# Optimization experiments

Measured on AMD Instinct MI355X. Metric: run time of the kernel, lower is better.

Reference implementation:

```python
import jax, jax.numpy as jnp
import numpy as np

N_NODES = 100000
N_EDGES = 1600000
IN_DIM = 256
OUT_DIM = 128


def setup_inputs() -> dict:
    key = jax.random.key(0)
    k1, k2, k3, k4, k5 = jax.random.split(key, 5)
    h = jax.random.normal(k1, (N_NODES, IN_DIM), dtype=jnp.float32)
    # xavier_normal-ish scales for the two weight matrices
    W = jax.random.normal(k2, (IN_DIM, OUT_DIM), dtype=jnp.float32) * (2.0 / np.sqrt(IN_DIM + OUT_DIM))
    a = jax.random.normal(k3, (2 * OUT_DIM,), dtype=jnp.float32) * (2.0 / np.sqrt(2 * OUT_DIM + 1))
    src = jax.random.randint(k4, (N_EDGES,), 0, N_NODES, dtype=jnp.int32)
    dst = jax.random.randint(k5, (N_EDGES,), 0, N_NODES, dtype=jnp.int32)
    return {"h": h, "W": W, "a": a, "src": src, "dst": dst}


def reference(h, W, a, src, dst):
    n = h.shape[0]
    d = W.shape[1]
    z = h @ W  # [N, out_dim]
    # attn_fc([z_src || z_dst]) == z_src @ a[:d] + z_dst @ a[d:]
    el = z @ a[:d]  # [N]
    er = z @ a[d:]  # [N]
    e = jax.nn.leaky_relu(el[src] + er[dst])  # [E], torch default slope 0.01
    # per-destination (segment) softmax, numerically stable
    seg_max = jax.ops.segment_max(e, dst, num_segments=n)
    e_exp = jnp.exp(e - seg_max[dst])
    denom = jax.ops.segment_sum(e_exp, dst, num_segments=n)
    alpha = e_exp / denom[dst]  # [E]
    # weighted scatter-sum of source z into destinations
    h_out = jax.ops.segment_sum(alpha[:, None] * z[src], dst, num_segments=n)
    return h_out
```

## Files before the change

kernel.cpp:

```cpp
#include <hip/hip_runtime.h>
#include <cstdint>
#include <cstddef>

#define N_NODES 100000
#define N_EDGES 1600000
#define IN_DIM  256
#define OUT_DIM 128

#define BSHIFT 6
#define BNODES 64
#define NBUCK  1563
#define BCAP   1600
#define CNTMAX 1408
#define EPB    2048
#define PGB    2346

typedef __attribute__((ext_vector_type(8))) short bf16x8;
typedef __attribute__((ext_vector_type(4))) float f32x4;

__device__ __forceinline__ unsigned bf16rn(float f) {
    unsigned u = __float_as_uint(f);
    return (u + 0x7FFFu + ((u >> 16) & 1u)) >> 16;
}

__global__ __launch_bounds__(256) void setup_k(
    const float* __restrict__ W, unsigned short* __restrict__ w16s,
    int* __restrict__ bucket_cursor)
{
    int t = blockIdx.x * blockDim.x + threadIdx.x;
    if (t < NBUCK) bucket_cursor[t] = 0;
    if (t >= IN_DIM * OUT_DIM) return;
    int j  = t & 7;
    int n  = (t >> 3) & 15;
    int q  = (t >> 7) & 3;
    int c  = (t >> 9) & 7;
    int kc = t >> 12;
    int k   = kc * 32 + q * 8 + j;
    int dim = (c >> 1) * 32 + n * 2 + (c & 1);
    w16s[t] = (unsigned short)bf16rn(W[k * OUT_DIM + dim]);
}

__global__ __launch_bounds__(256, 3) void pg_k(
    const int* __restrict__ src, const int* __restrict__ dst,
    int* __restrict__ bucket_cursor, unsigned* __restrict__ ebuf,
    const float* __restrict__ h, const unsigned short* __restrict__ w16s,
    const float* __restrict__ a,
    unsigned short* __restrict__ z16, float* __restrict__ el, float* __restrict__ er)
{
    __shared__ int hist[NBUCK];
    __shared__ int gbaseL[NBUCK];
    const int t   = threadIdx.x;
    const int bid = blockIdx.x;

    if ((bid % 3) == 2) {
        const int pid = bid / 3;
        for (int i = t; i < NBUCK; i += 256) hist[i] = 0;
        __syncthreads();

        const int e0 = pid * EPB;
        int bucks[8], ranks[8];
        unsigned pk[8];
        #pragma unroll
        for (int k = 0; k < 8; ++k) {
            int e = e0 + k * 256 + t;
            bucks[k] = -1;
            if (e < N_EDGES) {
                int s = src[e], d = dst[e];
                int b = d >> BSHIFT;
                bucks[k] = b;
                ranks[k] = atomicAdd(&hist[b], 1);
                pk[k] = ((unsigned)s << BSHIFT) | (unsigned)(d & (BNODES - 1));
            }
        }
        __syncthreads();
        for (int i = t; i < NBUCK; i += 256) {
            int hc = hist[i];
            gbaseL[i] = hc ? atomicAdd(&bucket_cursor[i], hc) : 0;
        }
        __syncthreads();
        #pragma unroll
        for (int k = 0; k < 8; ++k)
            if (bucks[k] >= 0) {
                int p = gbaseL[bucks[k]] + ranks[k];
                if (p < BCAP)
                    ebuf[(size_t)bucks[k] * BCAP + p] = pk[k];
            }
        return;
    }

    const int gid  = (bid / 3) * 2 + (bid % 3);
    const int n0   = gid * 64;
    if (n0 >= N_NODES) return;
    const int w    = t >> 6;
    const int lane = t & 63;
    const int q    = lane >> 4;
    const int col  = lane & 15;

    int row  = n0 + w * 16 + col;
    int lrow = (row < N_NODES) ? row : (N_NODES - 1);
    const float* hp = h + (size_t)lrow * IN_DIM + q * 8;

    f32x4 acc[8];
    #pragma unroll
    for (int c = 0; c < 8; ++c) acc[c] = (f32x4){0.f, 0.f, 0.f, 0.f};

    #pragma unroll
    for (int kc = 0; kc < 8; ++kc) {
        float4 v0 = *(const float4*)(hp + kc * 32);
        float4 v1 = *(const float4*)(hp + kc * 32 + 4);
        bf16x8 af;
        af[0] = (short)bf16rn(v0.x); af[1] = (short)bf16rn(v0.y);
        af[2] = (short)bf16rn(v0.z); af[3] = (short)bf16rn(v0.w);
        af[4] = (short)bf16rn(v1.x); af[5] = (short)bf16rn(v1.y);
        af[6] = (short)bf16rn(v1.z); af[7] = (short)bf16rn(v1.w);
        #pragma unroll
        for (int c = 0; c < 8; ++c) {
            bf16x8 bfr = *(const bf16x8*)&w16s[((((kc * 8 + c) * 4 + q) * 16) + col) * 8];
            acc[c] = __builtin_amdgcn_mfma_f32_16x16x32_bf16(af, bfr, acc[c], 0, 0, 0);
        }
    }

    float aL[8], aR[8];
    #pragma unroll
    for (int c = 0; c < 8; ++c) {
        int dim = (c >> 1) * 32 + col * 2 + (c & 1);
        aL[c] = a[dim];
        aR[c] = a[128 + dim];
    }
    #pragma unroll
    for (int r = 0; r < 4; ++r) {
        int node = n0 + w * 16 + q * 4 + r;
        float sl = 0.f, sr = 0.f;
        #pragma unroll
        for (int c = 0; c < 8; ++c) {
            sl += acc[c][r] * aL[c];
            sr += acc[c][r] * aR[c];
        }
        #pragma unroll
        for (int o = 1; o < 16; o <<= 1) {
            sl += __shfl_xor(sl, o, 64);
            sr += __shfl_xor(sr, o, 64);
        }
        if (node < N_NODES) {
            #pragma unroll
            for (int g = 0; g < 4; ++g) {
                unsigned u = bf16rn(acc[2 * g][r]) | (bf16rn(acc[2 * g + 1][r]) << 16);
                ((unsigned*)z16)[(size_t)node * 64 + g * 16 + col] = u;
            }
            if (col == 0) { el[node] = sl; er[node] = sr; }
        }
    }
}

__global__ __launch_bounds__(512, 8) void bn_k(
    const int* __restrict__ bucket_cursor, const unsigned* __restrict__ ebuf,
    const float* __restrict__ el, const float* __restrict__ er,
    const unsigned* __restrict__ z16, float* __restrict__ out)
{
    __shared__ float erL[2 * BNODES];
    __shared__ int   degA[BNODES], offA[BNODES];
    __shared__ int   degB[BNODES], offB[BNODES];
    __shared__ unsigned long long wsA[BCAP], wsB[BCAP];

    const int blk = blockIdx.x;
    const int t   = threadIdx.x;
    const int bA  = blk * 2;
    const int bB  = blk * 2 + 1;
    const bool hasB = (bB < NBUCK);

    int cA = bucket_cursor[bA]; if (cA > CNTMAX) cA = CNTMAX;
    int cB = 0;
    if (hasB) { cB = bucket_cursor[bB]; if (cB > CNTMAX) cB = CNTMAX; }

    if (t < BNODES) { degA[t] = 0; degB[t] = 0; }
    if (t < 2 * BNODES) {
        int bucket = (t < BNODES) ? bA : bB;
        int n = bucket * BNODES + (t & (BNODES - 1));
        erL[t] = (bucket < NBUCK && n < N_NODES) ? er[n] : 0.f;
    }
    __syncthreads();

    const int iA = 4 * t;
    unsigned evsA[4] = {0u, 0u, 0u, 0u};
    float wA[4]; int rkA[4];
    if (iA < cA) {
        uint4 v = *(const uint4*)&ebuf[(size_t)bA * BCAP + iA];
        evsA[0] = v.x; evsA[1] = v.y; evsA[2] = v.z; evsA[3] = v.w;
    }
    {
        float eg[4];
        #pragma unroll
        for (int j = 0; j < 4; ++j)
            eg[j] = (iA + j < cA) ? el[evsA[j] >> BSHIFT] : 0.f;
        #pragma unroll
        for (int j = 0; j < 4; ++j) {
            if (iA + j < cA) {
                int ld = evsA[j] & (BNODES - 1);
                float e = eg[j] + erL[ld];
                e = (e > 0.f) ? e : 0.01f * e;
                wA[j]  = __expf(e);
                rkA[j] = atomicAdd(&degA[ld], 1);
            }
        }
    }
    __syncthreads();

    if (t < BNODES) {
        int d = degA[t], pd = (d + 3) & ~3, incl = pd;
        #pragma unroll
        for (int o = 1; o < 64; o <<= 1) {
            int x = __shfl_up(incl, o, 64);
            if (t >= o) incl += x;
        }
        offA[t] = incl - pd;
    }
    __syncthreads();

    #pragma unroll
    for (int j = 0; j < 4; ++j)
        if (iA + j < cA) {
            int ld = evsA[j] & (BNODES - 1);
            wsA[offA[ld] + rkA[j]] =
                ((unsigned long long)__float_as_uint(wA[j]) << 32) | (evsA[j] >> BSHIFT);
        }
    if (t < BNODES) {
        int d = degA[t], pd = (d + 3) & ~3, o = offA[t];
        for (int j = o + d; j < o + pd; ++j) wsA[j] = 0ull;
    }
    __syncthreads();

    unsigned evsB[4] = {0u, 0u, 0u, 0u};
    float wB[4]; int rkB[4];
    if (iA < cB) {
        uint4 v = *(const uint4*)&ebuf[(size_t)bB * BCAP + iA];
        evsB[0] = v.x; evsB[1] = v.y; evsB[2] = v.z; evsB[3] = v.w;
    }
    {
        float eg[4];
        #pragma unroll
        for (int j = 0; j < 4; ++j)
            eg[j] = (iA + j < cB) ? el[evsB[j] >> BSHIFT] : 0.f;
        #pragma unroll
        for (int j = 0; j < 4; ++j) {
            if (iA + j < cB) {
                int ld = evsB[j] & (BNODES - 1);
                float e = eg[j] + erL[BNODES + ld];
                e = (e > 0.f) ? e : 0.01f * e;
                wB[j]  = __expf(e);
                rkB[j] = atomicAdd(&degB[ld], 1);
            }
        }
    }

    const int wv   = t >> 6;
    const int lane = t & 63;
    #pragma unroll 1
    for (int k = 0; k < BNODES / 8; ++k) {
        int ln = wv * (BNODES / 8) + k;
        int n  = bA * BNODES + ln;
        if (n >= N_NODES) continue;
        int o   = offA[ln];
        int dl  = degA[ln];
        int pdl = (dl + 3) & ~3;
        float acc0 = 0.f, acc1 = 0.f, dsum = 0.f;
        #pragma unroll 2
        for (int i = o; i < o + pdl; i += 4) {
            unsigned long long e0 = wsA[i],     e1 = wsA[i + 1];
            unsigned long long e2 = wsA[i + 2], e3 = wsA[i + 3];
            float w0 = __uint_as_float((unsigned)(e0 >> 32));
            float w1 = __uint_as_float((unsigned)(e1 >> 32));
            float w2 = __uint_as_float((unsigned)(e2 >> 32));
            float w3 = __uint_as_float((unsigned)(e3 >> 32));
            unsigned q0 = z16[(size_t)(unsigned)e0 * 64 + lane];
            unsigned q1 = z16[(size_t)(unsigned)e1 * 64 + lane];
            unsigned q2 = z16[(size_t)(unsigned)e2 * 64 + lane];
            unsigned q3 = z16[(size_t)(unsigned)e3 * 64 + lane];
            acc0 += w0 * __uint_as_float(q0 << 16)
                  + w1 * __uint_as_float(q1 << 16)
                  + w2 * __uint_as_float(q2 << 16)
                  + w3 * __uint_as_float(q3 << 16);
            acc1 += w0 * __uint_as_float(q0 & 0xFFFF0000u)
                  + w1 * __uint_as_float(q1 & 0xFFFF0000u)
                  + w2 * __uint_as_float(q2 & 0xFFFF0000u)
                  + w3 * __uint_as_float(q3 & 0xFFFF0000u);
            dsum += w0 + w1 + w2 + w3;
        }
        if (pdl > 0) {
            float inv = 1.0f / dsum;
            acc0 *= inv; acc1 *= inv;
        }
        *(float2*)&out[(size_t)n * OUT_DIM + lane * 2] = make_float2(acc0, acc1);
    }
    __syncthreads();

    if (t < BNODES) {
        int d = degB[t], pd = (d + 3) & ~3, incl = pd;
        #pragma unroll
        for (int o = 1; o < 64; o <<= 1) {
            int x = __shfl_up(incl, o, 64);
            if (t >= o) incl += x;
        }
        offB[t] = incl - pd;
    }
    __syncthreads();

    #pragma unroll
    for (int j = 0; j < 4; ++j)
        if (iA + j < cB) {
            int ld = evsB[j] & (BNODES - 1);
            wsB[offB[ld] + rkB[j]] =
                ((unsigned long long)__float_as_uint(wB[j]) << 32) | (evsB[j] >> BSHIFT);
        }
    if (t < BNODES) {
        int d = degB[t], pd = (d + 3) & ~3, o = offB[t];
        for (int j = o + d; j < o + pd; ++j) wsB[j] = 0ull;
    }
    __syncthreads();

    if (hasB) {
        #pragma unroll 1
        for (int k = 0; k < BNODES / 8; ++k) {
            int ln = wv * (BNODES / 8) + k;
            int n  = bB * BNODES + ln;
            if (n >= N_NODES) continue;
            int o   = offB[ln];
            int dl  = degB[ln];
            int pdl = (dl + 3) & ~3;
            float acc0 = 0.f, acc1 = 0.f, dsum = 0.f;
            #pragma unroll 2
            for (int i = o; i < o + pdl; i += 4) {
                unsigned long long e0 = wsB[i],     e1 = wsB[i + 1];
                unsigned long long e2 = wsB[i + 2], e3 = wsB[i + 3];
                float w0 = __uint_as_float((unsigned)(e0 >> 32));
                float w1 = __uint_as_float((unsigned)(e1 >> 32));
                float w2 = __uint_as_float((unsigned)(e2 >> 32));
                float w3 = __uint_as_float((unsigned)(e3 >> 32));
                unsigned q0 = z16[(size_t)(unsigned)e0 * 64 + lane];
                unsigned q1 = z16[(size_t)(unsigned)e1 * 64 + lane];
                unsigned q2 = z16[(size_t)(unsigned)e2 * 64 + lane];
                unsigned q3 = z16[(size_t)(unsigned)e3 * 64 + lane];
                acc0 += w0 * __uint_as_float(q0 << 16)
                      + w1 * __uint_as_float(q1 << 16)
                      + w2 * __uint_as_float(q2 << 16)
                      + w3 * __uint_as_float(q3 << 16);
                acc1 += w0 * __uint_as_float(q0 & 0xFFFF0000u)
                      + w1 * __uint_as_float(q1 & 0xFFFF0000u)
                      + w2 * __uint_as_float(q2 & 0xFFFF0000u)
                      + w3 * __uint_as_float(q3 & 0xFFFF0000u);
                dsum += w0 + w1 + w2 + w3;
            }
            if (pdl > 0) {
                float inv = 1.0f / dsum;
                acc0 *= inv; acc1 *= inv;
            }
            *(float2*)&out[(size_t)n * OUT_DIM + lane * 2] = make_float2(acc0, acc1);
        }
    }
}

extern "C" void kernel_launch(void* const* d_in, const int* in_sizes, int n_in,
                              void* d_out, int out_size, void* d_ws, size_t ws_size,
                              hipStream_t stream)
{
    (void)in_sizes; (void)n_in; (void)out_size; (void)ws_size;
    const float* h = (const float*)d_in[0];
    const float* W = (const float*)d_in[1];
    const float* a = (const float*)d_in[2];
    const int* src = (const int*)d_in[3];
    const int* dst = (const int*)d_in[4];
    float* out = (float*)d_out;

    char* ws = (char*)d_ws;
    size_t off = 0;
    auto alloc = [&](size_t bytes) -> char* {
        char* p = ws + off;
        off += (bytes + 255) & ~(size_t)255;
        return p;
    };
    unsigned short* z16  = (unsigned short*)alloc((size_t)N_NODES * OUT_DIM * 2);
    unsigned short* w16s = (unsigned short*)alloc((size_t)IN_DIM * OUT_DIM * 2);
    float*    el        = (float*)   alloc((size_t)N_NODES * 4);
    float*    er        = (float*)   alloc((size_t)N_NODES * 4);
    int*      bucket_cursor = (int*) alloc((size_t)NBUCK * 4);
    unsigned* ebuf      = (unsigned*)alloc((size_t)NBUCK * BCAP * 4);

    setup_k<<<(IN_DIM * OUT_DIM + 255) / 256, 256, 0, stream>>>(W, w16s, bucket_cursor);
    pg_k<<<PGB, 256, 0, stream>>>(src, dst, bucket_cursor, ebuf,
                                  h, w16s, a, z16, el, er);
    bn_k<<<(NBUCK + 1) / 2, 512, 0, stream>>>(bucket_cursor, ebuf, el, er,
                                              (const unsigned*)z16, out);
}
```

Baseline: 287.6 us.

## Split fp32-to-bf16 h conversion from GEMM into separate pass before partitioning

The fused projection+partition kernel is replaced by a kernel that converts h to a bf16 copy, builds the edge buckets and converts W, followed by a separate GEMM kernel that reads the bf16 h and preloads all A fragments. The bucket cursor reset moves to a memset. The intent is to overlap the bandwidth-bound h conversion with edge partitioning and to let the GEMM load half the bytes with loads issued ahead of the MFMA chain. In exchange it adds an extra 51 MB write and read of h16, plus one more kernel launch.

```diff
diff --git a/kernel.cpp b/kernel.cpp
--- a/kernel.cpp
+++ b/kernel.cpp
@@ -13,7 +13,10 @@
 #define BCAP   1600
 #define CNTMAX 1408
 #define EPB    2048
-#define PGB    2346
+#define NH16   1564
+#define NPART  782
+#define NW16   128
+#define PHPB   (NH16 + NPART + NW16)
 
 typedef __attribute__((ext_vector_type(8))) short bf16x8;
 typedef __attribute__((ext_vector_type(4))) float f32x4;
@@ -23,34 +26,29 @@
     return (u + 0x7FFFu + ((u >> 16) & 1u)) >> 16;
 }
 
-__global__ __launch_bounds__(256) void setup_k(
-    const float* __restrict__ W, unsigned short* __restrict__ w16s,
-    int* __restrict__ bucket_cursor)
-{
-    int t = blockIdx.x * blockDim.x + threadIdx.x;
-    if (t < NBUCK) bucket_cursor[t] = 0;
-    if (t >= IN_DIM * OUT_DIM) return;
-    int j  = t & 7;
-    int n  = (t >> 3) & 15;
-    int q  = (t >> 7) & 3;
-    int c  = (t >> 9) & 7;
-    int kc = t >> 12;
-    int k   = kc * 32 + q * 8 + j;
-    int dim = (c >> 1) * 32 + n * 2 + (c & 1);
-    w16s[t] = (unsigned short)bf16rn(W[k * OUT_DIM + dim]);
-}
-
-__global__ __launch_bounds__(256, 3) void pg_k(
+__global__ __launch_bounds__(256) void php_k(
+    const float* __restrict__ h, unsigned short* __restrict__ h16,
     const int* __restrict__ src, const int* __restrict__ dst,
     int* __restrict__ bucket_cursor, unsigned* __restrict__ ebuf,
-    const float* __restrict__ h, const unsigned short* __restrict__ w16s,
-    const float* __restrict__ a,
-    unsigned short* __restrict__ z16, float* __restrict__ el, float* __restrict__ er)
+    const float* __restrict__ W, unsigned short* __restrict__ w16s)
 {
     __shared__ int hist[NBUCK];
     __shared__ int gbaseL[NBUCK];
     const int t   = threadIdx.x;
     const int bid = blockIdx.x;
+
+    if (bid >= NH16 + NPART) {
+        int tt = (bid - (NH16 + NPART)) * 256 + t;
+        int j  = tt & 7;
+        int n  = (tt >> 3) & 15;
+        int q  = (tt >> 7) & 3;
+        int c  = (tt >> 9) & 7;
+        int kc = tt >> 12;
+        int k   = kc * 32 + q * 8 + j;
+        int dim = (c >> 1) * 32 + n * 2 + (c & 1);
+        w16s[tt] = (unsigned short)bf16rn(W[k * OUT_DIM + dim]);
+        return;
+    }
 
     if ((bid % 3) == 2) {
         const int pid = bid / 3;
@@ -88,8 +86,31 @@
         return;
     }
 
-    const int gid  = (bid / 3) * 2 + (bid % 3);
-    const int n0   = gid * 64;
+    const int gid = (bid / 3) * 2 + (bid % 3);
+    #pragma unroll
+    for (int jj = 0; jj < 8; ++jj) {
+        size_t base = (size_t)gid * 16384 + jj * 2048 + t * 8;
+        if (base < (size_t)N_NODES * IN_DIM) {
+            float4 v0 = *(const float4*)&h[base];
+            float4 v1 = *(const float4*)&h[base + 4];
+            uint2 lo, hi;
+            lo.x = bf16rn(v0.x) | (bf16rn(v0.y) << 16);
+            lo.y = bf16rn(v0.z) | (bf16rn(v0.w) << 16);
+            hi.x = bf16rn(v1.x) | (bf16rn(v1.y) << 16);
+            hi.y = bf16rn(v1.z) | (bf16rn(v1.w) << 16);
+            *(uint2*)&h16[base]     = lo;
+            *(uint2*)&h16[base + 4] = hi;
+        }
+    }
+}
+
+__global__ __launch_bounds__(256, 3) void gemm_k(
+    const unsigned short* __restrict__ h16, const unsigned short* __restrict__ w16s,
+    const float* __restrict__ a,
+    unsigned short* __restrict__ z16, float* __restrict__ el, float* __restrict__ er)
+{
+    const int t    = threadIdx.x;
+    const int n0   = blockIdx.x * 64;
     if (n0 >= N_NODES) return;
     const int w    = t >> 6;
     const int lane = t & 63;
@@ -98,7 +119,12 @@
 
     int row  = n0 + w * 16 + col;
     int lrow = (row < N_NODES) ? row : (N_NODES - 1);
-    const float* hp = h + (size_t)lrow * IN_DIM + q * 8;
+    const unsigned short* hp = h16 + (size_t)lrow * IN_DIM + q * 8;
+
+    bf16x8 vh[8];
+    #pragma unroll
+    for (int kc = 0; kc < 8; ++kc)
+        vh[kc] = *(const bf16x8*)&hp[kc * 32];
 
     f32x4 acc[8];
     #pragma unroll
@@ -106,17 +132,10 @@
 
     #pragma unroll
     for (int kc = 0; kc < 8; ++kc) {
-        float4 v0 = *(const float4*)(hp + kc * 32);
-        float4 v1 = *(const float4*)(hp + kc * 32 + 4);
-        bf16x8 af;
-        af[0] = (short)bf16rn(v0.x); af[1] = (short)bf16rn(v0.y);
-        af[2] = (short)bf16rn(v0.z); af[3] = (short)bf16rn(v0.w);
-        af[4] = (short)bf16rn(v1.x); af[5] = (short)bf16rn(v1.y);
-        af[6] = (short)bf16rn(v1.z); af[7] = (short)bf16rn(v1.w);
         #pragma unroll
         for (int c = 0; c < 8; ++c) {
             bf16x8 bfr = *(const bf16x8*)&w16s[((((kc * 8 + c) * 4 + q) * 16) + col) * 8];
-            acc[c] = __builtin_amdgcn_mfma_f32_16x16x32_bf16(af, bfr, acc[c], 0, 0, 0);
+            acc[c] = __builtin_amdgcn_mfma_f32_16x16x32_bf16(vh[kc], bfr, acc[c], 0, 0, 0);
         }
     }
 
@@ -378,15 +397,16 @@
         return p;
     };
     unsigned short* z16  = (unsigned short*)alloc((size_t)N_NODES * OUT_DIM * 2);
+    unsigned short* h16  = (unsigned short*)alloc((size_t)N_NODES * IN_DIM * 2);
     unsigned short* w16s = (unsigned short*)alloc((size_t)IN_DIM * OUT_DIM * 2);
     float*    el        = (float*)   alloc((size_t)N_NODES * 4);
     float*    er        = (float*)   alloc((size_t)N_NODES * 4);
     int*      bucket_cursor = (int*) alloc((size_t)NBUCK * 4);
     unsigned* ebuf      = (unsigned*)alloc((size_t)NBUCK * BCAP * 4);
 
-    setup_k<<<(IN_DIM * OUT_DIM + 255) / 256, 256, 0, stream>>>(W, w16s, bucket_cursor);
-    pg_k<<<PGB, 256, 0, stream>>>(src, dst, bucket_cursor, ebuf,
-                                  h, w16s, a, z16, el, er);
+    hipMemsetAsync(bucket_cursor, 0, (size_t)NBUCK * 4, stream);
+    php_k<<<PHPB, 256, 0, stream>>>(h, h16, src, dst, bucket_cursor, ebuf, W, w16s);
+    gemm_k<<<1564, 256, 0, stream>>>(h16, w16s, a, z16, el, er);
     bn_k<<<(NBUCK + 1) / 2, 512, 0, stream>>>(bucket_cursor, ebuf, el, er,
                                               (const unsigned*)z16, out);
 }
```

Result: slower. 307.4 us (+6.9%).

## Split fused partition/GEMM kernel and stage bf16 weights in LDS

Applied to the files above, without the earlier changes.

Separates the combined edge-partition and node-projection kernel into two kernels, a partition kernel followed by a GEMM kernel. The GEMM kernel now uses 512-thread blocks of 128 nodes and copies the full 64KB bf16 weight matrix into shared memory, so MFMA operands come from LDS instead of repeated global/L2 loads. This gives up the overlap between partitioning and GEMM that the fused kernel provided, adds an extra launch, and the 64KB of LDS per block limits occupancy.

```diff
diff --git a/kernel.cpp b/kernel.cpp
--- a/kernel.cpp
+++ b/kernel.cpp
@@ -13,7 +13,8 @@
 #define BCAP   1600
 #define CNTMAX 1408
 #define EPB    2048
-#define PGB    2346
+#define NPART  782
+#define NGEMM  782
 
 typedef __attribute__((ext_vector_type(8))) short bf16x8;
 typedef __attribute__((ext_vector_type(4))) float f32x4;
@@ -28,7 +29,7 @@
     int* __restrict__ bucket_cursor)
 {
     int t = blockIdx.x * blockDim.x + threadIdx.x;
-    if (t < NBUCK) bucket_cursor[t] = 0;
+    for (int i = t; i < NBUCK; i += 128 * 256) bucket_cursor[i] = 0;
     if (t >= IN_DIM * OUT_DIM) return;
     int j  = t & 7;
     int n  = (t >> 3) & 15;
@@ -40,63 +41,70 @@
     w16s[t] = (unsigned short)bf16rn(W[k * OUT_DIM + dim]);
 }
 
-__global__ __launch_bounds__(256, 3) void pg_k(
+__global__ __launch_bounds__(256) void part_k(
     const int* __restrict__ src, const int* __restrict__ dst,
-    int* __restrict__ bucket_cursor, unsigned* __restrict__ ebuf,
+    int* __restrict__ bucket_cursor, unsigned* __restrict__ ebuf)
+{
+    __shared__ int hist[NBUCK];
+    __shared__ int gbaseL[NBUCK];
+    const int t = threadIdx.x;
+    for (int i = t; i < NBUCK; i += 256) hist[i] = 0;
+    __syncthreads();
+
+    const int e0 = blockIdx.x * EPB;
+    int bucks[8], ranks[8];
+    unsigned pk[8];
+    #pragma unroll
+    for (int k = 0; k < 8; ++k) {
+        int e = e0 + k * 256 + t;
+        bucks[k] = -1;
+        if (e < N_EDGES) {
+            int s = src[e], d = dst[e];
+            int b = d >> BSHIFT;
+            bucks[k] = b;
+            ranks[k] = atomicAdd(&hist[b], 1);
+            pk[k] = ((unsigned)s << BSHIFT) | (unsigned)(d & (BNODES - 1));
+        }
+    }
+    __syncthreads();
+    for (int i = t; i < NBUCK; i += 256) {
+        int hc = hist[i];
+        gbaseL[i] = hc ? atomicAdd(&bucket_cursor[i], hc) : 0;
+    }
+    __syncthreads();
+    #pragma unroll
+    for (int k = 0; k < 8; ++k)
+        if (bucks[k] >= 0) {
+            int p = gbaseL[bucks[k]] + ranks[k];
+            if (p < BCAP)
+                ebuf[(size_t)bucks[k] * BCAP + p] = pk[k];
+        }
+}
+
+__global__ __launch_bounds__(512, 4) void gemm_k(
     const float* __restrict__ h, const unsigned short* __restrict__ w16s,
     const float* __restrict__ a,
     unsigned short* __restrict__ z16, float* __restrict__ el, float* __restrict__ er)
 {
-    __shared__ int hist[NBUCK];
-    __shared__ int gbaseL[NBUCK];
-    const int t   = threadIdx.x;
-    const int bid = blockIdx.x;
-
-    if ((bid % 3) == 2) {
-        const int pid = bid / 3;
-        for (int i = t; i < NBUCK; i += 256) hist[i] = 0;
-        __syncthreads();
-
-        const int e0 = pid * EPB;
-        int bucks[8], ranks[8];
-        unsigned pk[8];
-        #pragma unroll
-        for (int k = 0; k < 8; ++k) {
-            int e = e0 + k * 256 + t;
-            bucks[k] = -1;
-            if (e < N_EDGES) {
-                int s = src[e], d = dst[e];
-                int b = d >> BSHIFT;
-                bucks[k] = b;
-                ranks[k] = atomicAdd(&hist[b], 1);
-                pk[k] = ((unsigned)s << BSHIFT) | (unsigned)(d & (BNODES - 1));
-            }
-        }
-        __syncthreads();
-        for (int i = t; i < NBUCK; i += 256) {
-            int hc = hist[i];
-            gbaseL[i] = hc ? atomicAdd(&bucket_cursor[i], hc) : 0;
-        }
-        __syncthreads();
-        #pragma unroll
-        for (int k = 0; k < 8; ++k)
-            if (bucks[k] >= 0) {
-                int p = gbaseL[bucks[k]] + ranks[k];
-                if (p < BCAP)
-                    ebuf[(size_t)bucks[k] * BCAP + p] = pk[k];
-            }
-        return;
-    }
-
-    const int gid  = (bid / 3) * 2 + (bid % 3);
-    const int n0   = gid * 64;
-    if (n0 >= N_NODES) return;
-    const int w    = t >> 6;
+    __shared__ unsigned short lW[IN_DIM * OUT_DIM];
+
+    const int t = threadIdx.x;
+    {
+        const uint4* wsrc = (const uint4*)w16s;
+        uint4* wdst = (uint4*)lW;
+        #pragma unroll
+        for (int i = 0; i < 8; ++i)
+            wdst[i * 512 + t] = wsrc[i * 512 + t];
+    }
+    __syncthreads();
+
+    const int n0   = blockIdx.x * 128;
+    const int wv   = t >> 6;
     const int lane = t & 63;
     const int q    = lane >> 4;
     const int col  = lane & 15;
 
-    int row  = n0 + w * 16 + col;
+    int row  = n0 + wv * 16 + col;
     int lrow = (row < N_NODES) ? row : (N_NODES - 1);
     const float* hp = h + (size_t)lrow * IN_DIM + q * 8;
 
@@ -115,7 +123,7 @@
         af[6] = (short)bf16rn(v1.z); af[7] = (short)bf16rn(v1.w);
         #pragma unroll
         for (int c = 0; c < 8; ++c) {
-            bf16x8 bfr = *(const bf16x8*)&w16s[((((kc * 8 + c) * 4 + q) * 16) + col) * 8];
+            bf16x8 bfr = *(const bf16x8*)&lW[((((kc * 8 + c) * 4 + q) * 16) + col) * 8];
             acc[c] = __builtin_amdgcn_mfma_f32_16x16x32_bf16(af, bfr, acc[c], 0, 0, 0);
         }
     }
@@ -129,7 +137,7 @@
     }
     #pragma unroll
     for (int r = 0; r < 4; ++r) {
-        int node = n0 + w * 16 + q * 4 + r;
+        int node = n0 + wv * 16 + q * 4 + r;
         float sl = 0.f, sr = 0.f;
         #pragma unroll
         for (int c = 0; c < 8; ++c) {
@@ -384,9 +392,9 @@
     int*      bucket_cursor = (int*) alloc((size_t)NBUCK * 4);
     unsigned* ebuf      = (unsigned*)alloc((size_t)NBUCK * BCAP * 4);
 
-    setup_k<<<(IN_DIM * OUT_DIM + 255) / 256, 256, 0, stream>>>(W, w16s, bucket_cursor);
-    pg_k<<<PGB, 256, 0, stream>>>(src, dst, bucket_cursor, ebuf,
-                                  h, w16s, a, z16, el, er);
+    setup_k<<<128, 256, 0, stream>>>(W, w16s, bucket_cursor);
+    part_k<<<NPART, 256, 0, stream>>>(src, dst, bucket_cursor, ebuf);
+    gemm_k<<<NGEMM, 512, 0, stream>>>(h, w16s, a, z16, el, er);
     bn_k<<<(NBUCK + 1) / 2, 512, 0, stream>>>(bucket_cursor, ebuf, el, er,
                                               (const unsigned*)z16, out);
 }
```

Result: slower. 301.7 us (+4.9%).
